# Performance work log

Hardware: AMD Instinct MI355X
Metric: run time of the kernel (lower is better)

Reference implementation:

```python
import jax, jax.numpy as jnp
import numpy as np

INTERMEDIATE = 11008  # weight.size(0)
HIDDEN = 4096         # weight.size(1)
REMAINED = 4403       # int(11008 * 0.4)
BATCH = 64


def setup_inputs() -> dict:
    key = jax.random.key(0)
    k1, k2, k3 = jax.random.split(key, 3)
    x = jax.random.normal(k1, (BATCH, 1, HIDDEN), dtype=jnp.float32)
    weight = jax.random.normal(k2, (INTERMEDIATE, HIDDEN), dtype=jnp.float32) * 0.02
    indices = jax.random.randint(k3, (REMAINED,), 0, INTERMEDIATE, dtype=jnp.int32)
    return {"x": x, "weight": weight, "indices": indices}


def reference(x, weight, indices):
    # Decode path of UpLayer.forward: gather the activation-predicted neuron
    # rows into filtered_W, then x @ filtered_W.T  -> [B, 1, REMAINED]
    filtered_w = weight[indices]                      # [REMAINED, HIDDEN]
    return jnp.einsum('bsh,nh->bsn', x, filtered_w)   # [B, 1, REMAINED]
```

## Files before the change

### kernel.cpp

```cpp
#include <hip/hip_runtime.h>
#include <hip/hip_bf16.h>


#define HIDDEN 4096
#define KSPLIT 8
#define KCHUNK (HIDDEN / KSPLIT)
#define KSTEPS (KCHUNK / 32)
#define BATCH  64
#define NTILE  32
#define XBF_OFF (16u << 20)

using short8 = __attribute__((ext_vector_type(8))) short;
using f32x4  = __attribute__((ext_vector_type(4))) float;

typedef const void __attribute__((address_space(1))) gvoid;
typedef void __attribute__((address_space(3))) svoid;

__device__ __forceinline__ short f2bf(float f) {
    __bf16 h = (__bf16)f;
    return __builtin_bit_cast(short, h);
}

__device__ __forceinline__ short8 cvt8(const f32x4& lo, const f32x4& hi) {
    short8 r;
    r[0] = f2bf(lo[0]); r[1] = f2bf(lo[1]); r[2] = f2bf(lo[2]); r[3] = f2bf(lo[3]);
    r[4] = f2bf(hi[0]); r[5] = f2bf(hi[1]); r[6] = f2bf(hi[2]); r[7] = f2bf(hi[3]);
    return r;
}

__global__ __launch_bounds__(256) void cvt_x(
    const float* __restrict__ x, unsigned short* __restrict__ xbf)
{
    const int i = (blockIdx.x * 256 + threadIdx.x) * 8;
    f32x4 a = *(const f32x4*)(x + i);
    f32x4 b = *(const f32x4*)(x + i + 4);
    *(short8*)(xbf + i) = cvt8(a, b);
}

__global__ __launch_bounds__(256, 2) void gather_gemm(
    const float*          __restrict__ weight,
    const unsigned short* __restrict__ xbf,
    const int*            __restrict__ indices,
    float*                __restrict__ ws,
    int R)
{
    __shared__ float wlds[NTILE * KCHUNK];

    const int t    = threadIdx.x;
    const int lane = t & 63;
    const int wave = t >> 6;
    const int nl   = lane & 15;
    const int kg   = lane >> 4;
    const int nb   = blockIdx.x;
    const int kb   = blockIdx.y;
    const int k0   = kb * KCHUNK;

    {
        const int r0 = wave * 8;
#pragma unroll
        for (int j = 0; j < 8; ++j) {
            const int r = r0 + j;
            const int n = nb * NTILE + r;
            const int wrow = indices[n < R ? n : R - 1];
            const char* rowp = (const char*)(weight + (size_t)wrow * HIDDEN + k0);
            const unsigned int swz = (unsigned int)((r & 7) << 4);
#pragma unroll
            for (int h = 0; h < 2; ++h) {
                const unsigned int srcoff =
                    ((unsigned int)(h * 1024 + lane * 16)) ^ swz;
                __builtin_amdgcn_global_load_lds(
                    (gvoid*)(rowp + srcoff),
                    (svoid*)((char*)wlds + r * 2048 + h * 1024),
                    16, 0, 0);
            }
        }
    }

    const unsigned short* xrow =
        xbf + (size_t)(wave * 16 + nl) * HIDDEN + k0 + kg * 8;
    short8 afr[KSTEPS];
#pragma unroll
    for (int ks = 0; ks < KSTEPS; ++ks)
        afr[ks] = *(const short8*)(xrow + ks * 32);

    __syncthreads();

    f32x4 acc0 = {0.f,0.f,0.f,0.f}, acc1 = {0.f,0.f,0.f,0.f};

#pragma unroll
    for (int ks = 0; ks < KSTEPS; ++ks) {
#pragma unroll
        for (int nf = 0; nf < 2; ++nf) {
            const int rr = nf * 16 + nl;
            const unsigned int swz = (unsigned int)((rr & 7) << 4);
            const unsigned int g0 = (unsigned int)(ks * 128 + kg * 32);
            const char* rowbase = (const char*)wlds + rr * 2048;
            f32x4 w0 = *(const f32x4*)(rowbase + (g0 ^ swz));
            f32x4 w1 = *(const f32x4*)(rowbase + ((g0 + 16) ^ swz));
            short8 b = cvt8(w0, w1);
            f32x4& acc = nf == 0 ? acc0 : acc1;
            acc = __builtin_amdgcn_mfma_f32_16x16x32_bf16(afr[ks], b, acc, 0, 0, 0);
        }
    }

    float* part = ws + (size_t)kb * BATCH * R;
    f32x4 accs[2] = {acc0, acc1};
#pragma unroll
    for (int nf = 0; nf < 2; ++nf) {
        const int nn = nb * NTILE + nf * 16 + nl;
        if (nn < R) {
#pragma unroll
            for (int r = 0; r < 4; ++r) {
                const int brow = wave * 16 + kg * 4 + r;
                part[(size_t)brow * R + nn] = accs[nf][r];
            }
        }
    }
}

__global__ __launch_bounds__(256) void reduce_partials(
    const float* __restrict__ ws, float* __restrict__ out, int n4, int stride4)
{
    const int i = blockIdx.x * blockDim.x + threadIdx.x;
    if (i >= n4) return;
    const f32x4* w = (const f32x4*)ws;
    f32x4 s = __builtin_nontemporal_load(&w[i]);
#pragma unroll
    for (int kb = 1; kb < KSPLIT; ++kb) {
        f32x4 v = __builtin_nontemporal_load(&w[(size_t)kb * stride4 + i]);
        s[0] += v[0]; s[1] += v[1]; s[2] += v[2]; s[3] += v[3];
    }
    ((f32x4*)out)[i] = s;
}

extern "C" void kernel_launch(void* const* d_in, const int* in_sizes, int n_in,
                              void* d_out, int out_size, void* d_ws, size_t ws_size,
                              hipStream_t stream) {
    const float* x       = (const float*)d_in[0];
    const float* weight  = (const float*)d_in[1];
    const int*   indices = (const int*)d_in[2];
    float*       out     = (float*)d_out;
    float*       ws      = (float*)d_ws;
    unsigned short* xbf  = (unsigned short*)((char*)d_ws + XBF_OFF);

    const int R  = in_sizes[2];
    const int nb = (R + NTILE - 1) / NTILE;

    cvt_x<<<dim3((BATCH * HIDDEN) / (256 * 8)), dim3(256), 0, stream>>>(x, xbf);
    gather_gemm<<<dim3(nb, KSPLIT), dim3(256), 0, stream>>>(weight, xbf, indices, ws, R);

    const int n4 = (BATCH * R) / 4;
    reduce_partials<<<dim3((n4 + 255) / 256), dim3(256), 0, stream>>>(ws, out, n4, n4);
}
```

Before: 34.59 us.

## Double-buffer two K-chunks per block with 16-row N tiles in gather GEMM

The N tile shrinks from 32 to 16 gathered rows, and each block now processes two consecutive K chunks. The second chunk's weight rows are staged into a second LDS buffer while the first chunk is computed, so gather latency overlaps with compute. The LDS swizzle changes from 16-byte to 32-byte granularity to match the new read pattern, and the reduce kernel uses ordinary loads instead of nontemporal ones. The grid is now hardcoded to 276 N tiles, which ties it to R=4403. Each block carries more A-fragment registers, and the total block count stays about the same.

```diff
diff --git a/kernel.cpp b/kernel.cpp
--- a/kernel.cpp
+++ b/kernel.cpp
@@ -7,7 +7,8 @@
 #define KCHUNK (HIDDEN / KSPLIT)
 #define KSTEPS (KCHUNK / 32)
 #define BATCH  64
-#define NTILE  32
+#define NTILE  16
+#define NTILES 276
 #define XBF_OFF (16u << 20)
 
 using short8 = __attribute__((ext_vector_type(8))) short;
@@ -44,7 +45,7 @@
     float*                __restrict__ ws,
     int R)
 {
-    __shared__ float wlds[NTILE * KCHUNK];
+    __shared__ float wlds[2][NTILE * KCHUNK];
 
     const int t    = threadIdx.x;
     const int lane = t & 63;
@@ -52,70 +53,85 @@
     const int nl   = lane & 15;
     const int kg   = lane >> 4;
     const int nb   = blockIdx.x;
-    const int kb   = blockIdx.y;
-    const int k0   = kb * KCHUNK;
+    const int kb0  = blockIdx.y * 2;
+    const int kb1  = kb0 + 1;
 
-    {
-        const int r0 = wave * 8;
-#pragma unroll
-        for (int j = 0; j < 8; ++j) {
-            const int r = r0 + j;
-            const int n = nb * NTILE + r;
-            const int wrow = indices[n < R ? n : R - 1];
-            const char* rowp = (const char*)(weight + (size_t)wrow * HIDDEN + k0);
-            const unsigned int swz = (unsigned int)((r & 7) << 4);
-#pragma unroll
-            for (int h = 0; h < 2; ++h) {
-                const unsigned int srcoff =
-                    ((unsigned int)(h * 1024 + lane * 16)) ^ swz;
-                __builtin_amdgcn_global_load_lds(
-                    (gvoid*)(rowp + srcoff),
-                    (svoid*)((char*)wlds + r * 2048 + h * 1024),
-                    16, 0, 0);
-            }
-        }
+#define STAGE(buf, kb)                                                         \
+    {                                                                          \
+        _Pragma("unroll")                                                      \
+        for (int j = 0; j < 8; ++j) {                                          \
+            const int r = 4 * wave + (j >> 1);                                 \
+            const int h = j & 1;                                               \
+            const int n = nb * NTILE + r;                                      \
+            const int wrow = indices[n < R ? n : R - 1];                       \
+            const char* rowp =                                                 \
+                (const char*)(weight + (size_t)wrow * HIDDEN + (kb) * KCHUNK); \
+            const unsigned int srcoff =                                        \
+                ((unsigned int)(h * 1024 + lane * 16)) ^                       \
+                ((unsigned int)((r & 7) << 5));                                \
+            __builtin_amdgcn_global_load_lds(                                  \
+                (gvoid*)(rowp + srcoff),                                       \
+                (svoid*)((char*)wlds[buf] + r * 2048 + h * 1024), 16, 0, 0);   \
+        }                                                                      \
     }
 
+#define COMPUTE(buf, afr, acc)                                                 \
+    {                                                                          \
+        _Pragma("unroll")                                                      \
+        for (int ks = 0; ks < KSTEPS; ++ks) {                                  \
+            const unsigned int g0 = (unsigned int)(ks * 128 + kg * 32);        \
+            const unsigned int off = g0 ^ ((unsigned int)((nl & 7) << 5));     \
+            const char* rowbase = (const char*)wlds[buf] + nl * 2048;          \
+            f32x4 w0 = *(const f32x4*)(rowbase + off);                         \
+            f32x4 w1 = *(const f32x4*)(rowbase + off + 16);                    \
+            short8 b = cvt8(w0, w1);                                           \
+            acc = __builtin_amdgcn_mfma_f32_16x16x32_bf16(afr[ks], b, acc,     \
+                                                          0, 0, 0);            \
+        }                                                                      \
+    }
+
+#define STORE(kb, acc)                                                         \
+    {                                                                          \
+        const int nn = nb * NTILE + nl;                                        \
+        if (nn < R) {                                                          \
+            float* p = ws + (size_t)(kb) * BATCH * R;                          \
+            _Pragma("unroll")                                                  \
+            for (int r = 0; r < 4; ++r) {                                      \
+                const int brow = wave * 16 + kg * 4 + r;                       \
+                p[(size_t)brow * R + nn] = acc[r];                             \
+            }                                                                  \
+        }                                                                      \
+    }
+
+    STAGE(0, kb0);
+
     const unsigned short* xrow =
-        xbf + (size_t)(wave * 16 + nl) * HIDDEN + k0 + kg * 8;
-    short8 afr[KSTEPS];
+        xbf + (size_t)(wave * 16 + nl) * HIDDEN + kg * 8;
+    short8 afrA[KSTEPS], afrB[KSTEPS];
 #pragma unroll
     for (int ks = 0; ks < KSTEPS; ++ks)
-        afr[ks] = *(const short8*)(xrow + ks * 32);
+        afrA[ks] = *(const short8*)(xrow + kb0 * KCHUNK + ks * 32);
+#pragma unroll
+    for (int ks = 0; ks < KSTEPS; ++ks)
+        afrB[ks] = *(const short8*)(xrow + kb1 * KCHUNK + ks * 32);
 
     __syncthreads();
 
-    f32x4 acc0 = {0.f,0.f,0.f,0.f}, acc1 = {0.f,0.f,0.f,0.f};
+    STAGE(1, kb1);
 
-#pragma unroll
-    for (int ks = 0; ks < KSTEPS; ++ks) {
-#pragma unroll
-        for (int nf = 0; nf < 2; ++nf) {
-            const int rr = nf * 16 + nl;
-            const unsigned int swz = (unsigned int)((rr & 7) << 4);
-            const unsigned int g0 = (unsigned int)(ks * 128 + kg * 32);
-            const char* rowbase = (const char*)wlds + rr * 2048;
-            f32x4 w0 = *(const f32x4*)(rowbase + (g0 ^ swz));
-            f32x4 w1 = *(const f32x4*)(rowbase + ((g0 + 16) ^ swz));
-            short8 b = cvt8(w0, w1);
-            f32x4& acc = nf == 0 ? acc0 : acc1;
-            acc = __builtin_amdgcn_mfma_f32_16x16x32_bf16(afr[ks], b, acc, 0, 0, 0);
-        }
-    }
+    f32x4 acc0 = {0.f, 0.f, 0.f, 0.f};
+    COMPUTE(0, afrA, acc0);
+    STORE(kb0, acc0);
 
-    float* part = ws + (size_t)kb * BATCH * R;
-    f32x4 accs[2] = {acc0, acc1};
-#pragma unroll
-    for (int nf = 0; nf < 2; ++nf) {
-        const int nn = nb * NTILE + nf * 16 + nl;
-        if (nn < R) {
-#pragma unroll
-            for (int r = 0; r < 4; ++r) {
-                const int brow = wave * 16 + kg * 4 + r;
-                part[(size_t)brow * R + nn] = accs[nf][r];
-            }
-        }
-    }
+    __syncthreads();
+
+    f32x4 acc1 = {0.f, 0.f, 0.f, 0.f};
+    COMPUTE(1, afrB, acc1);
+    STORE(kb1, acc1);
+
+#undef STAGE
+#undef COMPUTE
+#undef STORE
 }
 
 __global__ __launch_bounds__(256) void reduce_partials(
@@ -124,10 +140,10 @@
     const int i = blockIdx.x * blockDim.x + threadIdx.x;
     if (i >= n4) return;
     const f32x4* w = (const f32x4*)ws;
-    f32x4 s = __builtin_nontemporal_load(&w[i]);
+    f32x4 s = w[i];
 #pragma unroll
     for (int kb = 1; kb < KSPLIT; ++kb) {
-        f32x4 v = __builtin_nontemporal_load(&w[(size_t)kb * stride4 + i]);
+        f32x4 v = w[(size_t)kb * stride4 + i];
         s[0] += v[0]; s[1] += v[1]; s[2] += v[2]; s[3] += v[3];
     }
     ((f32x4*)out)[i] = s;
@@ -143,11 +159,11 @@
     float*       ws      = (float*)d_ws;
     unsigned short* xbf  = (unsigned short*)((char*)d_ws + XBF_OFF);
 
-    const int R  = in_sizes[2];
-    const int nb = (R + NTILE - 1) / NTILE;
+    const int R = in_sizes[2];
 
     cvt_x<<<dim3((BATCH * HIDDEN) / (256 * 8)), dim3(256), 0, stream>>>(x, xbf);
-    gather_gemm<<<dim3(nb, KSPLIT), dim3(256), 0, stream>>>(weight, xbf, indices, ws, R);
+    gather_gemm<<<dim3(NTILES, KSPLIT / 2), dim3(256), 0, stream>>>(
+        weight, xbf, indices, ws, R);
 
     const int n4 = (BATCH * R) / 4;
     reduce_partials<<<dim3((n4 + 255) / 256), dim3(256), 0, stream>>>(ws, out, n4, n4);
```

Measured after the change: 42.85 us. 1.24x slower.
